# Kernel tuning notes

Hardware: AMD Instinct MI355X
Metric: run time of the kernel (lower is better)

## Reference

```python
import jax, jax.numpy as jnp
import numpy as np
import math

C = 256

def conv_bn_lrelu(x, w, scale, bias, dilation):
    # Conv2d(k=3, stride=1, padding=dilation, dilation=dilation, bias=False) + eval BN (folded) + LeakyReLU(0.1)
    d = dilation
    y = jax.lax.conv_general_dilated(
        x, w, window_strides=(1, 1), padding=[(d, d), (d, d)],
        rhs_dilation=(d, d), dimension_numbers=('NCHW', 'OIHW', 'NCHW'))
    y = y * scale[None, :, None, None] + bias[None, :, None, None]
    return jnp.where(y > 0, y, 0.1 * y)

def unfold3x3(x):
    # [b,c,h,w] -> [b,c,9,h,w]: 3x3 neighborhoods (zero pad 1), row-major window order like F.unfold
    b, c, h, w = x.shape
    xp = jnp.pad(x, ((0, 0), (0, 0), (1, 1), (1, 1)))
    return jnp.stack([xp[:, :, i:i + h, j:j + w] for i in range(3) for j in range(3)], axis=2)

def self_attn(Q, K, V):
    b, c, h, w = Q.shape
    Ku = unfold3x3(K)                     # [b,c,9,h,w]
    Vu = unfold3x3(V)                     # [b,c,9,h,w]
    dot = Q[:, :, None] * Ku * (1.0 / math.sqrt(c))
    dot = jax.nn.softmax(dot, axis=2)     # softmax over 9 neighbors, per channel
    return jnp.sum(dot * Vu, axis=2)      # [b,c,h,w]

def setup_inputs() -> dict:
    key = jax.random.key(0)
    ks = jax.random.split(key, 20)
    fan = C * 9
    wstd = math.sqrt(2.0 / fan)
    def w(k):
        return jax.random.normal(k, (C, C, 3, 3), dtype=jnp.float32) * wstd
    def s(k):
        return jax.random.uniform(k, (C,), dtype=jnp.float32, minval=0.5, maxval=1.5)
    def b(k):
        return jax.random.normal(k, (C,), dtype=jnp.float32) * 0.1
    inp = {'x': jax.random.normal(ks[0], (4, C, 64, 64), dtype=jnp.float32)}
    names = ['q1', 'k1', 'v1', 'q2', 'k2', 'v2']
    for i, n in enumerate(names):
        inp[n[0] + 'w' + n[1]] = w(ks[1 + 3 * i])
        inp[n[0] + 's' + n[1]] = s(ks[2 + 3 * i])
        inp[n[0] + 'b' + n[1]] = b(ks[3 + 3 * i])
    return inp

def reference(x, qw1, qs1, qb1, kw1, ks1, kb1, vw1, vs1, vb1,
              qw2, qs2, qb2, kw2, ks2, kb2, vw2, vs2, vb2):
    Q1 = conv_bn_lrelu(x, qw1, qs1, qb1, dilation=1)
    K1 = conv_bn_lrelu(x, kw1, ks1, kb1, dilation=1)
    V1 = conv_bn_lrelu(x, vw1, vs1, vb1, dilation=1)
    attn1 = self_attn(Q1, K1, V1)
    Q2 = conv_bn_lrelu(attn1, qw2, qs2, qb2, dilation=2)
    K2 = conv_bn_lrelu(attn1, kw2, ks2, kb2, dilation=2)
    V2 = conv_bn_lrelu(attn1, vw2, vs2, vb2, dilation=2)
    return self_attn(Q2, K2, V2)
```

## Files before the change

### kernel.cpp

```cpp
#include <hip/hip_runtime.h>
#include <stdint.h>

typedef __attribute__((ext_vector_type(8))) short short8;
typedef __attribute__((ext_vector_type(4))) float f32x4;
typedef __attribute__((ext_vector_type(4))) unsigned short u16x4;
typedef __attribute__((ext_vector_type(8))) unsigned short u16x8;

#define DEV static __device__ __forceinline__

DEV unsigned short f2bf(float f) {
  unsigned u = __float_as_uint(f);
  u += 0x7FFFu + ((u >> 16) & 1u);
  return (unsigned short)(u >> 16);
}
DEV float bf2f(unsigned short s) { return __uint_as_float(((unsigned)s) << 16); }

DEV void gload16(const void* g, void* l) {
  __attribute__((address_space(1))) unsigned* gp =
      reinterpret_cast<__attribute__((address_space(1))) unsigned*>(
          reinterpret_cast<uintptr_t>(g));
  __attribute__((address_space(3))) unsigned* lp =
      reinterpret_cast<__attribute__((address_space(3))) unsigned*>(
          reinterpret_cast<uintptr_t>(l));
  __builtin_amdgcn_global_load_lds(gp, lp, 16, 0, 0);
}

__global__ __launch_bounds__(256) void prep_w6(
    const float* __restrict__ w0, const float* __restrict__ s0,
    const float* __restrict__ w1, const float* __restrict__ s1,
    const float* __restrict__ w2, const float* __restrict__ s2,
    const float* __restrict__ w3, const float* __restrict__ s3,
    const float* __restrict__ w4, const float* __restrict__ s4,
    const float* __restrict__ w5, const float* __restrict__ s5,
    unsigned short* __restrict__ W2base) {
  const int set = blockIdx.y;
  const float* wl[6] = {w0, w1, w2, w3, w4, w5};
  const float* sl[6] = {s0, s1, s2, s3, s4, s5};
  const int cout = blockIdx.x;
  const int t = threadIdx.x;
  const float sc = sl[set][cout];
  const float* src = wl[set] + ((size_t)cout * 256 + t) * 9;
  float v[9];
#pragma unroll
  for (int k = 0; k < 9; ++k) v[k] = src[k] * sc;
  unsigned short* dst =
      W2base + (size_t)set * 256 * 2304 + (size_t)cout * 2304;
#pragma unroll
  for (int k = 0; k < 9; ++k) dst[k * 256 + t] = f2bf(v[k]);
}

__global__ __launch_bounds__(256) void zero_borders(
    unsigned short* __restrict__ XP, unsigned short* __restrict__ QP,
    unsigned short* __restrict__ KP, unsigned short* __restrict__ VP,
    unsigned short* __restrict__ AP) {
  const int buf = blockIdx.y >> 2, b = blockIdx.y & 3;
  const int P = (buf == 4) ? 68 : 66;
  const int pad = (buf == 4) ? 2 : 1;
  const int nb = P * P - 64 * 64;
  const int i = blockIdx.x * 256 + threadIdx.x;
  const int pxi = i >> 5, ch = (i & 31) * 8;
  if (pxi >= nb) return;
  const int topbot = 2 * pad * P;
  int h, w;
  if (pxi < topbot) {
    const int r = pxi / P, c = pxi - r * P;
    h = (r < pad) ? r : P - 2 * pad + r;
    w = c;
  } else {
    const int j = pxi - topbot;
    const int r = j / (2 * pad), c = j - r * 2 * pad;
    h = pad + r;
    w = (c < pad) ? c : P - 2 * pad + c;
  }
  unsigned short* base = buf == 0 ? XP : buf == 1 ? QP : buf == 2 ? KP
                         : buf == 3 ? VP : AP;
  const u16x8 z = {0, 0, 0, 0, 0, 0, 0, 0};
  *(u16x8*)&base[((size_t)(b * P + h) * P + w) * 256 + ch] = z;
}

__global__ __launch_bounds__(256) void pad_cast(const float* __restrict__ x,
                                                unsigned short* __restrict__ Xp) {
  __shared__ float sm[64][65];
  const int bid = blockIdx.x;
  const int ct = bid & 3;
  const int h = (bid >> 2) & 63;
  const int b = bid >> 8;
  const int t = threadIdx.x;
  const int wl = t & 63, cr = t >> 6;
#pragma unroll
  for (int cc = 0; cc < 16; ++cc) {
    const int c = cc * 4 + cr;
    sm[c][wl] = x[((size_t)(b * 256 + ct * 64 + c) * 64 + h) * 64 + wl];
  }
  __syncthreads();
  const int ww = t >> 2, c16 = (t & 3) * 16;
  u16x8 o0, o1;
#pragma unroll
  for (int i = 0; i < 8; ++i) o0[i] = f2bf(sm[c16 + i][ww]);
#pragma unroll
  for (int i = 0; i < 8; ++i) o1[i] = f2bf(sm[c16 + 8 + i][ww]);
  const size_t base =
      ((size_t)(b * 66 + h + 1) * 66 + (ww + 1)) * 256 + ct * 64 + c16;
  *(u16x8*)&Xp[base] = o0;
  *(u16x8*)&Xp[base + 8] = o1;
}

template <int D>
__global__ __launch_bounds__(256, 2) void conv_qkv(
    const unsigned short* __restrict__ Xp, const unsigned short* __restrict__ Wq,
    const unsigned short* __restrict__ Wk, const unsigned short* __restrict__ Wv,
    const float* __restrict__ bq, const float* __restrict__ bk,
    const float* __restrict__ bv, unsigned short* __restrict__ Qo,
    unsigned short* __restrict__ Ko, unsigned short* __restrict__ Vo) {
  constexpr int P = 64 + 2 * D;
  constexpr int HALF = 128 * 64 + 3 * 64 * 64;
  __shared__ __align__(16) unsigned short lds[2 * HALF];

  const int tid = threadIdx.x;
  const int lane = tid & 63;
  const int wid = tid >> 6;
  const int wm = wid >> 1;
  const int wn = wid & 1;
  const int wgid = blockIdx.x;
  const int xcd = wgid & 7;
  const int m0 = (xcd & 3) * 64;
  const int rg = (wgid >> 3) + 64 * (xcd >> 2);
  const int b = rg >> 5;
  const int h0 = (rg & 31) * 2;

  f32x4 acc[3][2][4];
#pragma unroll
  for (int c = 0; c < 3; ++c)
#pragma unroll
    for (int m = 0; m < 2; ++m)
#pragma unroll
      for (int n = 0; n < 4; ++n) acc[c][m][n] = (f32x4){0.f, 0.f, 0.f, 0.f};

  const int w0i = tid >> 3;
  const int j3 = (tid & 7) ^ (w0i & 7);
  const unsigned short* wptr[3] = {Wq, Wk, Wv};
  size_t bRow[2];
#pragma unroll
  for (int r = 0; r < 2; ++r)
    bRow[r] = ((size_t)(b * P + h0 + r) * P + w0i) * 256 + j3 * 8;
  const size_t aBase = (size_t)(m0 + w0i) * 2304 + j3 * 8;

  auto STAGE = [&](int s, int hf) {
    const int t = s >> 2, kb = s & 3;
    const int ty = t / 3, tx = t - ty * 3;
    const size_t tapOff = ((size_t)(ty * D) * P + tx * D) * 256 + kb * 64;
    const int kOff = t * 256 + kb * 64;
    unsigned short* base = &lds[hf * HALF];
#pragma unroll
    for (int k = 0; k < 4; ++k)
      gload16(Xp + bRow[k >> 1] + (size_t)(32 * (k & 1)) * 256 + tapOff,
              &base[(k * 256 + tid) * 8]);
#pragma unroll
    for (int k = 0; k < 6; ++k)
      gload16(wptr[k >> 1] + aBase + (size_t)(k & 1) * 32 * 2304 + kOff,
              &base[8192 + (k * 256 + tid) * 8]);
  };

  auto COMPUTE = [&](int hf) {
    const unsigned short* base = &lds[hf * HALF];
#pragma unroll
    for (int kk = 0; kk < 2; ++kk) {
      const int jc = kk * 4 + (lane >> 4);
      short8 bfr[4], afr[3][2];
#pragma unroll
      for (int n = 0; n < 4; ++n) {
        const int row = wn * 64 + n * 16 + (lane & 15);
        bfr[n] = *(const short8*)&base[row * 64 + ((jc ^ (row & 7)) << 3)];
      }
#pragma unroll
      for (int c = 0; c < 3; ++c)
#pragma unroll
        for (int m = 0; m < 2; ++m) {
          const int row = wm * 32 + m * 16 + (lane & 15);
          afr[c][m] = *(const short8*)&base[8192 + c * 4096 + row * 64 +
                                            ((jc ^ (row & 7)) << 3)];
        }
      __builtin_amdgcn_s_setprio(1);
#pragma unroll
      for (int c = 0; c < 3; ++c)
#pragma unroll
        for (int m = 0; m < 2; ++m)
#pragma unroll
          for (int n = 0; n < 4; ++n)
            acc[c][m][n] = __builtin_amdgcn_mfma_f32_16x16x32_bf16(
                afr[c][m], bfr[n], acc[c][m][n], 0, 0, 0);
      __builtin_amdgcn_s_setprio(0);
    }
  };

  STAGE(0, 0);
#pragma unroll 1
  for (int s = 0; s < 35; ++s) {
    const int p = s & 1;
    STAGE(s + 1, p ^ 1);
    asm volatile("s_waitcnt vmcnt(10)" ::: "memory");
    __builtin_amdgcn_s_barrier();
    COMPUTE(p);
    __builtin_amdgcn_s_barrier();
  }
  asm volatile("s_waitcnt vmcnt(0)" ::: "memory");
  __builtin_amdgcn_s_barrier();
  COMPUTE(1);

  const float* bias[3] = {bq, bk, bv};
  unsigned short* outp[3] = {Qo, Ko, Vo};
  const int r4 = (lane >> 4) << 2;
#pragma unroll
  for (int c = 0; c < 3; ++c) {
#pragma unroll
    for (int m = 0; m < 2; ++m) {
      const int cout = m0 + wm * 32 + m * 16 + r4;
      const f32x4 bb = *(const f32x4*)&bias[c][cout];
#pragma unroll
      for (int n = 0; n < 4; ++n) {
        const int px = wn * 64 + n * 16 + (lane & 15);
        const int ww = px & 63;
        const int hh = h0 + (px >> 6);
        const size_t off =
            ((size_t)(b * 66 + hh + 1) * 66 + (ww + 1)) * 256 + cout;
        u16x4 pk;
#pragma unroll
        for (int r = 0; r < 4; ++r) {
          float f = acc[c][m][n][r] + bb[r];
          f = f > 0.f ? f : 0.1f * f;
          pk[r] = f2bf(f);
        }
        *(u16x4*)&outp[c][off] = pk;
      }
    }
  }
}

template <int MODE>
__global__ __launch_bounds__(256) void attn3x3(
    const unsigned short* __restrict__ Qp, const unsigned short* __restrict__ Kp,
    const unsigned short* __restrict__ Vp, unsigned short* __restrict__ outB,
    float* __restrict__ outF) {
  __shared__ float so[8][257];
  const int tid = threadIdx.x;
  const int bid = ((blockIdx.x & 7) << 8) + (blockIdx.x >> 3);
  const int gid = bid * 256 + tid;
  const int cch = gid & 31;
  const int pix = gid >> 5;
  const int b = pix >> 12, h = (pix >> 6) & 63, w = pix & 63;
  const int c0 = cch * 8;

  const size_t cen = ((size_t)(b * 66 + h + 1) * 66 + (w + 1)) * 256 + c0;
  const size_t tl = ((size_t)(b * 66 + h) * 66 + w) * 256 + c0;

  float q[8];
  {
    u16x8 u = *(const u16x8*)&Qp[cen];
#pragma unroll
    for (int i = 0; i < 8; ++i) q[i] = bf2f(u[i]) * 0.0625f;
  }
  float s[9][8];
#pragma unroll
  for (int t = 0; t < 9; ++t) {
    u16x8 u = *(const u16x8*)&Kp[tl + (size_t)((t / 3) * 66 + (t % 3)) * 256];
#pragma unroll
    for (int i = 0; i < 8; ++i) s[t][i] = q[i] * bf2f(u[i]);
  }
  float mx[8];
#pragma unroll
  for (int i = 0; i < 8; ++i) {
    float m = s[0][i];
#pragma unroll
    for (int t = 1; t < 9; ++t) m = fmaxf(m, s[t][i]);
    mx[i] = m;
  }
  float num[8], den[8];
#pragma unroll
  for (int i = 0; i < 8; ++i) { num[i] = 0.f; den[i] = 0.f; }
#pragma unroll
  for (int t = 0; t < 9; ++t) {
    u16x8 u = *(const u16x8*)&Vp[tl + (size_t)((t / 3) * 66 + (t % 3)) * 256];
#pragma unroll
    for (int i = 0; i < 8; ++i) {
      const float e = __expf(s[t][i] - mx[i]);
      den[i] += e;
      num[i] += e * bf2f(u[i]);
    }
  }

  if (MODE == 0) {
    u16x8 o;
#pragma unroll
    for (int i = 0; i < 8; ++i) o[i] = f2bf(num[i] / den[i]);
    *(u16x8*)&outB[((size_t)(b * 68 + h + 2) * 68 + (w + 2)) * 256 + c0] = o;
  } else {
    const int ps = tid >> 5;
#pragma unroll
    for (int i = 0; i < 8; ++i) so[ps][c0 + i] = num[i] / den[i];
    __syncthreads();
    const int pix0 = bid * 8;
    const int b2 = pix0 >> 12, h2 = (pix0 >> 6) & 63, w0 = pix0 & 63;
    const int c = tid;
    const size_t ob = (((size_t)b2 * 256 + c) * 64 + h2) * 64 + w0;
    f32x4 v0 = (f32x4){so[0][c], so[1][c], so[2][c], so[3][c]};
    f32x4 v1 = (f32x4){so[4][c], so[5][c], so[6][c], so[7][c]};
    *(f32x4*)&outF[ob] = v0;
    *(f32x4*)&outF[ob + 4] = v1;
  }
}

extern "C" void kernel_launch(void* const* d_in, const int* in_sizes, int n_in,
                              void* d_out, int out_size, void* d_ws,
                              size_t ws_size, hipStream_t stream) {
  (void)in_sizes; (void)n_in; (void)out_size; (void)ws_size;
  const float* x = (const float*)d_in[0];
  const float* wqs[6] = {(const float*)d_in[1],  (const float*)d_in[4],
                         (const float*)d_in[7],  (const float*)d_in[10],
                         (const float*)d_in[13], (const float*)d_in[16]};
  const float* scs[6] = {(const float*)d_in[2],  (const float*)d_in[5],
                         (const float*)d_in[8],  (const float*)d_in[11],
                         (const float*)d_in[14], (const float*)d_in[17]};
  const float* bq1 = (const float*)d_in[3];
  const float* bk1 = (const float*)d_in[6];
  const float* bv1 = (const float*)d_in[9];
  const float* bq2 = (const float*)d_in[12];
  const float* bk2 = (const float*)d_in[15];
  const float* bv2 = (const float*)d_in[18];

  char* ws = (char*)d_ws;
  const size_t SZ66 = (size_t)4 * 66 * 66 * 256 * 2;
  const size_t SZ68 = (size_t)4 * 68 * 68 * 256 * 2;
  unsigned short* XP = (unsigned short*)(ws);
  unsigned short* QP = (unsigned short*)(ws + SZ66);
  unsigned short* KP = (unsigned short*)(ws + 2 * SZ66);
  unsigned short* VP = (unsigned short*)(ws + 3 * SZ66);
  unsigned short* AP = (unsigned short*)(ws + 4 * SZ66);
  const size_t wbase = 4 * SZ66 + SZ68;
  unsigned short* W2base = (unsigned short*)(ws + wbase);
  const size_t WSET = (size_t)256 * 2304;

  zero_borders<<<dim3(66, 20), 256, 0, stream>>>(XP, QP, KP, VP, AP);
  prep_w6<<<dim3(256, 6), 256, 0, stream>>>(
      wqs[0], scs[0], wqs[1], scs[1], wqs[2], scs[2], wqs[3], scs[3], wqs[4],
      scs[4], wqs[5], scs[5], W2base);
  pad_cast<<<1024, 256, 0, stream>>>(x, XP);

  conv_qkv<1><<<512, 256, 0, stream>>>(
      XP, W2base, W2base + WSET, W2base + 2 * WSET, bq1, bk1, bv1, QP, KP, VP);
  attn3x3<0><<<2048, 256, 0, stream>>>(QP, KP, VP, AP, nullptr);
  conv_qkv<2><<<512, 256, 0, stream>>>(
      AP, W2base + 3 * WSET, W2base + 4 * WSET, W2base + 5 * WSET, bq2, bk2,
      bv2, QP, KP, VP);
  attn3x3<1><<<2048, 256, 0, stream>>>(QP, KP, VP, nullptr, (float*)d_out);
}
```

Measured before the change: 163.7 us.

## Enlarge conv tile to 4 rows with 512 threads and interleave loads with MFMA phases

The fused QKV conv block grows from 256 to 512 threads and covers 4 output rows (256 pixels) per block instead of 2. Each weight tile loaded into LDS is therefore reused across twice as many pixels, and the grid shrinks to 256 blocks. The main loop splits each K-step into four phases that alternate LDS fragment reads, staged global-to-LDS prefetches and MFMA groups, separated by barriers and lgkmcnt fences, so memory traffic overlaps compute in finer pieces. The cost is doubled LDS per block (about 112 KB for two buffers), which may leave room for only one block per CU despite launch_bounds(512,2), plus many more barriers per iteration. The grid mapping also drops the XCD-aware block swizzle.

Result: slower. 168.7 us (+3.1%).

```diff
diff --git a/kernel.cpp b/kernel.cpp
--- a/kernel.cpp
+++ b/kernel.cpp
@@ -106,27 +106,25 @@
 }
 
 template <int D>
-__global__ __launch_bounds__(256, 2) void conv_qkv(
+__global__ __launch_bounds__(512, 2) void conv_qkv(
     const unsigned short* __restrict__ Xp, const unsigned short* __restrict__ Wq,
     const unsigned short* __restrict__ Wk, const unsigned short* __restrict__ Wv,
     const float* __restrict__ bq, const float* __restrict__ bk,
     const float* __restrict__ bv, unsigned short* __restrict__ Qo,
     unsigned short* __restrict__ Ko, unsigned short* __restrict__ Vo) {
   constexpr int P = 64 + 2 * D;
-  constexpr int HALF = 128 * 64 + 3 * 64 * 64;
+  constexpr int HALF = 256 * 64 + 3 * 64 * 64;
   __shared__ __align__(16) unsigned short lds[2 * HALF];
 
   const int tid = threadIdx.x;
   const int lane = tid & 63;
   const int wid = tid >> 6;
-  const int wm = wid >> 1;
-  const int wn = wid & 1;
-  const int wgid = blockIdx.x;
-  const int xcd = wgid & 7;
-  const int m0 = (xcd & 3) * 64;
-  const int rg = (wgid >> 3) + 64 * (xcd >> 2);
-  const int b = rg >> 5;
-  const int h0 = (rg & 31) * 2;
+  const int wm = wid >> 2;
+  const int wn = wid & 3;
+  const int m0 = blockIdx.x * 64;
+  const int rg = blockIdx.y;
+  const int b = rg >> 4;
+  const int h0 = (rg & 15) * 4;
 
   f32x4 acc[3][2][4];
 #pragma unroll
@@ -136,76 +134,115 @@
 #pragma unroll
       for (int n = 0; n < 4; ++n) acc[c][m][n] = (f32x4){0.f, 0.f, 0.f, 0.f};
 
-  const int w0i = tid >> 3;
-  const int j3 = (tid & 7) ^ (w0i & 7);
+  const int col = tid >> 3;
+  const int j3 = (tid & 7) ^ (col & 7);
   const unsigned short* wptr[3] = {Wq, Wk, Wv};
-  size_t bRow[2];
-#pragma unroll
-  for (int r = 0; r < 2; ++r)
-    bRow[r] = ((size_t)(b * P + h0 + r) * P + w0i) * 256 + j3 * 8;
-  const size_t aBase = (size_t)(m0 + w0i) * 2304 + j3 * 8;
-
-  auto STAGE = [&](int s, int hf) {
+  const size_t aBase = (size_t)(m0 + col) * 2304 + j3 * 8;
+  const size_t bBase0 = ((size_t)(b * P + h0) * P + col) * 256 + j3 * 8;
+  const int ldsOff = tid * 8;
+
+  auto GL = [&](int s, int c0, int c1, int hf) {
     const int t = s >> 2, kb = s & 3;
     const int ty = t / 3, tx = t - ty * 3;
     const size_t tapOff = ((size_t)(ty * D) * P + tx * D) * 256 + kb * 64;
     const int kOff = t * 256 + kb * 64;
     unsigned short* base = &lds[hf * HALF];
 #pragma unroll
-    for (int k = 0; k < 4; ++k)
-      gload16(Xp + bRow[k >> 1] + (size_t)(32 * (k & 1)) * 256 + tapOff,
-              &base[(k * 256 + tid) * 8]);
-#pragma unroll
-    for (int k = 0; k < 6; ++k)
-      gload16(wptr[k >> 1] + aBase + (size_t)(k & 1) * 32 * 2304 + kOff,
-              &base[8192 + (k * 256 + tid) * 8]);
+    for (int c = c0; c < c1; ++c) {
+      if (c < 4)
+        gload16(Xp + bBase0 + (size_t)c * P * 256 + tapOff,
+                &base[ldsOff + c * 4096]);
+      else
+        gload16(wptr[c - 4] + aBase + kOff,
+                &base[16384 + (c - 4) * 4096 + ldsOff]);
+    }
   };
 
-  auto COMPUTE = [&](int hf) {
-    const unsigned short* base = &lds[hf * HALF];
-#pragma unroll
-    for (int kk = 0; kk < 2; ++kk) {
-      const int jc = kk * 4 + (lane >> 4);
-      short8 bfr[4], afr[3][2];
-#pragma unroll
-      for (int n = 0; n < 4; ++n) {
-        const int row = wn * 64 + n * 16 + (lane & 15);
-        bfr[n] = *(const short8*)&base[row * 64 + ((jc ^ (row & 7)) << 3)];
-      }
-#pragma unroll
-      for (int c = 0; c < 3; ++c)
-#pragma unroll
-        for (int m = 0; m < 2; ++m) {
-          const int row = wm * 32 + m * 16 + (lane & 15);
-          afr[c][m] = *(const short8*)&base[8192 + c * 4096 + row * 64 +
-                                            ((jc ^ (row & 7)) << 3)];
-        }
-      __builtin_amdgcn_s_setprio(1);
-#pragma unroll
-      for (int c = 0; c < 3; ++c)
-#pragma unroll
-        for (int m = 0; m < 2; ++m)
-#pragma unroll
-          for (int n = 0; n < 4; ++n)
-            acc[c][m][n] = __builtin_amdgcn_mfma_f32_16x16x32_bf16(
-                afr[c][m], bfr[n], acc[c][m][n], 0, 0, 0);
-      __builtin_amdgcn_s_setprio(0);
+  auto RD_B = [&](short8* bfr, int kk, const unsigned short* base) {
+    const int jc = kk * 4 + (lane >> 4);
+#pragma unroll
+    for (int n = 0; n < 4; ++n) {
+      const int row = wn * 64 + n * 16 + (lane & 15);
+      bfr[n] = *(const short8*)&base[row * 64 + ((jc ^ (row & 7)) << 3)];
     }
   };
-
-  STAGE(0, 0);
+  auto RD_A = [&](short8* afr, int c, int kk, const unsigned short* base) {
+    const int jc = kk * 4 + (lane >> 4);
+#pragma unroll
+    for (int m = 0; m < 2; ++m) {
+      const int row = wm * 32 + m * 16 + (lane & 15);
+      afr[m] = *(const short8*)&base[16384 + c * 4096 + row * 64 +
+                                     ((jc ^ (row & 7)) << 3)];
+    }
+  };
+  auto MFMA8 = [&](int c, const short8* afr, const short8* bfr) {
+#pragma unroll
+    for (int m = 0; m < 2; ++m)
+#pragma unroll
+      for (int n = 0; n < 4; ++n)
+        acc[c][m][n] = __builtin_amdgcn_mfma_f32_16x16x32_bf16(
+            afr[m], bfr[n], acc[c][m][n], 0, 0, 0);
+  };
+
+#define LGKM0_FENCE                                   \
+  asm volatile("s_waitcnt lgkmcnt(0)" ::: "memory"); \
+  __builtin_amdgcn_sched_barrier(0)
+
+  GL(0, 0, 7, 0);
 #pragma unroll 1
-  for (int s = 0; s < 35; ++s) {
+  for (int s = 0; s < 36; ++s) {
     const int p = s & 1;
-    STAGE(s + 1, p ^ 1);
-    asm volatile("s_waitcnt vmcnt(10)" ::: "memory");
-    __builtin_amdgcn_s_barrier();
-    COMPUTE(p);
-    __builtin_amdgcn_s_barrier();
-  }
-  asm volatile("s_waitcnt vmcnt(0)" ::: "memory");
-  __builtin_amdgcn_s_barrier();
-  COMPUTE(1);
+    const unsigned short* base = &lds[p * HALF];
+    const bool last = (s == 35);
+    if (!last) {
+      GL(s + 1, 0, 2, p ^ 1);
+      asm volatile("s_waitcnt vmcnt(2)" ::: "memory");
+    } else {
+      asm volatile("s_waitcnt vmcnt(0)" ::: "memory");
+    }
+    __builtin_amdgcn_sched_barrier(0);
+    __builtin_amdgcn_s_barrier();
+
+    short8 bfr[4], a0[2], a1[2], a2[2];
+    RD_B(bfr, 0, base);
+    RD_A(a0, 0, 0, base);
+    if (!last) GL(s + 1, 2, 4, p ^ 1);
+    __builtin_amdgcn_s_barrier();
+    LGKM0_FENCE;
+    __builtin_amdgcn_s_setprio(1);
+    MFMA8(0, a0, bfr);
+    __builtin_amdgcn_s_setprio(0);
+    __builtin_amdgcn_s_barrier();
+    RD_A(a1, 1, 0, base);
+    RD_A(a2, 2, 0, base);
+    if (!last) GL(s + 1, 4, 6, p ^ 1);
+    __builtin_amdgcn_s_barrier();
+    LGKM0_FENCE;
+    __builtin_amdgcn_s_setprio(1);
+    MFMA8(1, a1, bfr);
+    MFMA8(2, a2, bfr);
+    __builtin_amdgcn_s_setprio(0);
+    __builtin_amdgcn_s_barrier();
+    RD_B(bfr, 1, base);
+    RD_A(a0, 0, 1, base);
+    if (!last) GL(s + 1, 6, 7, p ^ 1);
+    __builtin_amdgcn_s_barrier();
+    LGKM0_FENCE;
+    __builtin_amdgcn_s_setprio(1);
+    MFMA8(0, a0, bfr);
+    __builtin_amdgcn_s_setprio(0);
+    __builtin_amdgcn_s_barrier();
+    RD_A(a1, 1, 1, base);
+    RD_A(a2, 2, 1, base);
+    __builtin_amdgcn_s_barrier();
+    LGKM0_FENCE;
+    __builtin_amdgcn_s_setprio(1);
+    MFMA8(1, a1, bfr);
+    MFMA8(2, a2, bfr);
+    __builtin_amdgcn_s_setprio(0);
+    __builtin_amdgcn_s_barrier();
+  }
+#undef LGKM0_FENCE
 
   const float* bias[3] = {bq, bk, bv};
   unsigned short* outp[3] = {Qo, Ko, Vo};
@@ -345,10 +382,10 @@
       scs[4], wqs[5], scs[5], W2base);
   pad_cast<<<1024, 256, 0, stream>>>(x, XP);
 
-  conv_qkv<1><<<512, 256, 0, stream>>>(
+  conv_qkv<1><<<dim3(4, 64), 512, 0, stream>>>(
       XP, W2base, W2base + WSET, W2base + 2 * WSET, bq1, bk1, bv1, QP, KP, VP);
   attn3x3<0><<<2048, 256, 0, stream>>>(QP, KP, VP, AP, nullptr);
-  conv_qkv<2><<<512, 256, 0, stream>>>(
+  conv_qkv<2><<<dim3(4, 64), 512, 0, stream>>>(
       AP, W2base + 3 * WSET, W2base + 4 * WSET, W2base + 5 * WSET, bq2, bk2,
       bv2, QP, KP, VP);
   attn3x3<1><<<2048, 256, 0, stream>>>(QP, KP, VP, nullptr, (float*)d_out);
```
